# Kernel tuning notes

Measured on AMD Instinct MI355X. Metric: run time of the kernel, lower is better.

## Reference

```python
import jax, jax.numpy as jnp
import numpy as np

N = 100000
IN_C = 128
HID = 32   # 2*out_channels
OUT = 16
NEG_SLOPE = 0.2


def gat_layer(x, src, dst, n, W, a_src, a_dst, b):
    # x: [n, Cin] -> h: [n, Cout]
    h = x @ W
    alpha_s = h @ a_src  # [n]
    alpha_d = h @ a_dst  # [n]
    e = jax.nn.leaky_relu(alpha_s[src] + alpha_d[dst], NEG_SLOPE)  # [E]
    # softmax over edges grouped by destination node (self-loops ensure no empty groups)
    m = jax.ops.segment_max(e, dst, num_segments=n)
    ex = jnp.exp(e - m[dst])
    s = jax.ops.segment_sum(ex, dst, num_segments=n)
    alpha = ex / s[dst]  # [E]
    out = jax.ops.segment_sum(h[src] * alpha[:, None], dst, num_segments=n)
    return out + b


def setup_inputs() -> dict:
    key = jax.random.key(0)
    ks = jax.random.split(key, 16)
    x = jax.random.normal(ks[0], (N, IN_C), dtype=jnp.float32)
    edge_index = jax.random.randint(ks[1], (2, 1600000), 0, N, dtype=jnp.int64)

    def glorot(k, shape):
        fan = shape[0] + (shape[1] if len(shape) > 1 else 1)
        return jax.random.normal(k, shape, dtype=jnp.float32) * jnp.sqrt(2.0 / fan)

    return {
        "x": x,
        "edge_index": edge_index,
        "W1": glorot(ks[2], (IN_C, HID)),
        "a1_src": glorot(ks[3], (HID,)),
        "a1_dst": glorot(ks[4], (HID,)),
        "b1": jnp.zeros((HID,), dtype=jnp.float32),
        "W_mu": glorot(ks[5], (HID, OUT)),
        "a_mu_src": glorot(ks[6], (OUT,)),
        "a_mu_dst": glorot(ks[7], (OUT,)),
        "b_mu": jnp.zeros((OUT,), dtype=jnp.float32),
        "W_ls": glorot(ks[8], (HID, OUT)),
        "a_ls_src": glorot(ks[9], (OUT,)),
        "a_ls_dst": glorot(ks[10], (OUT,)),
        "b_ls": jnp.zeros((OUT,), dtype=jnp.float32),
    }


def reference(x, edge_index, W1, a1_src, a1_dst, b1,
              W_mu, a_mu_src, a_mu_dst, b_mu,
              W_ls, a_ls_src, a_ls_dst, b_ls):
    n = x.shape[0]
    # PyG GATConv default: add self-loops
    loop = jnp.arange(n, dtype=edge_index.dtype)
    src = jnp.concatenate([edge_index[0], loop])
    dst = jnp.concatenate([edge_index[1], loop])

    h = jax.nn.relu(gat_layer(x, src, dst, n, W1, a1_src, a1_dst, b1))
    mu = gat_layer(h, src, dst, n, W_mu, a_mu_src, a_mu_dst, b_mu)
    logstd = gat_layer(h, src, dst, n, W_ls, a_ls_src, a_ls_dst, b_ls)
    return (mu, logstd)
```

## Files before the change

### kernel.cpp

```cpp
#include <hip/hip_runtime.h>
#include <hip/hip_bf16.h>
#include <hip/hip_fp16.h>

typedef unsigned int u32;
typedef unsigned short u16;

__device__ __forceinline__ float lrelu(float v) {
    return v > 0.f ? v : 0.2f * v;
}

__device__ __forceinline__ float4 ldq_h16(const u16* __restrict__ row, int q) {
    uint2 u = ((const uint2*)row)[q];
    __half2 a = *(__half2*)&u.x;
    __half2 b = *(__half2*)&u.y;
    float2 fa = __half22float2(a);
    float2 fb = __half22float2(b);
    return make_float4(fa.x, fa.y, fb.x, fb.y);
}

__device__ __forceinline__ u32 pack2h(float x, float y) {
    __half2 h = __float22half2_rn(make_float2(x, y));
    return *(u32*)&h;
}

#define PCHUNK 4096
#define NW 256

__global__ __launch_bounds__(256) void g1p_kernel(
    const float* __restrict__ x, const float* __restrict__ W,
    const float* __restrict__ a_src, const float* __restrict__ a_dst,
    u16* __restrict__ h16, float* __restrict__ as_, float* __restrict__ ad_,
    const int* __restrict__ srcI, const int* __restrict__ dstI,
    u32* __restrict__ pairs, u32* __restrict__ bcur,
    int n, int E, int wsz, int cap, int pgrid)
{
    __shared__ float xs[64][132];
    __shared__ float Wl[128][32];
    __shared__ float asv[32], adv[32];
    __shared__ u32 lcount[NW];
    __shared__ u32 lbase[NW];
    int t = threadIdx.x;

    if ((int)blockIdx.x < pgrid) {
        int chunk = blockIdx.x * PCHUNK;
        lcount[t] = 0;
        __syncthreads();
        u32 pk[16]; int wv[16]; u32 rk[16]; bool val[16];
#pragma unroll
        for (int k = 0; k < 16; k++) {
            int i = chunk + k * 256 + t;
            val[k] = i < E;
            if (val[k]) {
                u32 s = (u32)srcI[i];
                u32 d = (u32)dstI[i];
                wv[k] = d / (u32)wsz;
                u32 dloc = d - (u32)wv[k] * (u32)wsz;
                pk[k] = (dloc << 17) | s;
                rk[k] = atomicAdd(&lcount[wv[k]], 1u);
            }
        }
        __syncthreads();
        if (lcount[t] > 0)
            lbase[t] = atomicAdd(&bcur[t], lcount[t]);
        __syncthreads();
#pragma unroll
        for (int k = 0; k < 16; k++) {
            if (val[k]) {
                u32 pos = lbase[wv[k]] + rk[k];
                if (pos < (u32)cap)
                    pairs[(size_t)wv[k] * cap + pos] = pk[k];
            }
        }
        return;
    }

    int rb = (blockIdx.x - pgrid) * 64;

    for (int i = t; i < 4096; i += 256) Wl[i >> 5][i & 31] = W[i];
    if (t < 32) { asv[t] = a_src[t]; adv[t] = a_dst[t]; }
    for (int i = t; i < 2048; i += 256) {
        int row = i >> 5, seg = i & 31;
        float4 v = make_float4(0.f, 0.f, 0.f, 0.f);
        if (rb + row < n)
            v = ((const float4*)(x + (size_t)(rb + row) * 128))[seg];
        int c = seg * 4;
        xs[row][c + 0] = v.x; xs[row][c + 1] = v.y;
        xs[row][c + 2] = v.z; xs[row][c + 3] = v.w;
    }
    __syncthreads();

    int tr = t >> 3;
    int tc = t & 7;
    float acc[2][4];
#pragma unroll
    for (int i = 0; i < 2; i++)
#pragma unroll
        for (int j = 0; j < 4; j++) acc[i][j] = 0.f;

#pragma unroll 4
    for (int k = 0; k < 128; k++) {
        float x0 = xs[tr][k];
        float x1 = xs[tr + 32][k];
        float4 wv = *(const float4*)&Wl[k][tc * 4];
        acc[0][0] += x0 * wv.x; acc[0][1] += x0 * wv.y;
        acc[0][2] += x0 * wv.z; acc[0][3] += x0 * wv.w;
        acc[1][0] += x1 * wv.x; acc[1][1] += x1 * wv.y;
        acc[1][2] += x1 * wv.z; acc[1][3] += x1 * wv.w;
    }

#pragma unroll
    for (int i = 0; i < 2; i++) {
        int r = rb + tr + i * 32;
        if (r < n) {
            uint2 p;
            p.x = pack2h(acc[i][0], acc[i][1]);
            p.y = pack2h(acc[i][2], acc[i][3]);
            *(uint2*)&h16[(size_t)r * 32 + tc * 4] = p;
        }
        float ps = 0.f, pd = 0.f;
#pragma unroll
        for (int j = 0; j < 4; j++) {
            int c = tc * 4 + j;
            ps += acc[i][j] * asv[c];
            pd += acc[i][j] * adv[c];
        }
        for (int m = 1; m < 8; m <<= 1) {
            ps += __shfl_xor(ps, m, 64);
            pd += __shfl_xor(pd, m, 64);
        }
        if (tc == 0 && r < n) { as_[r] = ps; ad_[r] = pd; }
    }
}

__global__ __launch_bounds__(256) void csr_window_kernel(
    const u32* __restrict__ pairs, const u32* __restrict__ bcur,
    u32* __restrict__ rowS, u32* __restrict__ deg, int* __restrict__ srcS,
    u32* __restrict__ perm,
    int n, int wsz, int cap)
{
    __shared__ u32 dw[512];
    __shared__ u32 cw[512];
    __shared__ u32 ts[256];
    __shared__ u32 hb[512];
    int grp = blockIdx.x;
    int t = threadIdx.x;
    int wlo = grp * wsz;
    int wnodes = n - wlo; if (wnodes < 0) wnodes = 0; if (wnodes > wsz) wnodes = wsz;
    u32 cnt = bcur[grp]; if (cnt > (u32)cap) cnt = (u32)cap;
    size_t base = (size_t)grp * cap;

    {
        int wlo_t = t * wsz;
        int wn_t = n - wlo_t; if (wn_t < 0) wn_t = 0; if (wn_t > wsz) wn_t = wsz;
        u32 c_t = bcur[t]; if (c_t > (u32)cap) c_t = (u32)cap;
        ts[t] = c_t + (u32)wn_t;
        __syncthreads();
        for (int o = 1; o < NW; o <<= 1) {
            u32 y = (t >= o) ? ts[t - o] : 0u;
            __syncthreads();
            ts[t] += y;
            __syncthreads();
        }
    }
    u32 wb = ts[grp] - (cnt + (u32)wnodes);
    __syncthreads();

    dw[t] = 0; dw[t + 256] = 0;
    hb[t] = 0; hb[t + 256] = 0;
    __syncthreads();
    for (u32 i = t; i < cnt; i += 256)
        atomicAdd(&dw[pairs[base + i] >> 17], 1u);
    __syncthreads();

    int i0 = 2 * t, i1 = 2 * t + 1;
    u32 e0 = (i0 < wnodes) ? dw[i0] + 1u : 0u;
    u32 e1 = (i1 < wnodes) ? dw[i1] + 1u : 0u;
    ts[t] = e0 + e1;
    __syncthreads();
    for (int o = 1; o < 256; o <<= 1) {
        u32 y = (t >= o) ? ts[t - o] : 0u;
        __syncthreads();
        ts[t] += y;
        __syncthreads();
    }
    u32 off = wb + ts[t] - (e0 + e1);
    if (i0 < wnodes) {
        u32 dgi = dw[i0];
        cw[i0] = off;
        rowS[wlo + i0] = off;
        deg[wlo + i0] = dgi;
        srcS[off + dgi] = wlo + i0;
    }
    u32 off1 = off + e0;
    if (i1 < wnodes) {
        u32 dgi = dw[i1];
        cw[i1] = off1;
        rowS[wlo + i1] = off1;
        deg[wlo + i1] = dgi;
        srcS[off1 + dgi] = wlo + i1;
    }
    __syncthreads();

    for (int i = t; i < wnodes; i += 256)
        atomicAdd(&hb[dw[i] < 511u ? dw[i] : 511u], 1u);
    __syncthreads();
    {
        u32 h0 = hb[2 * t], h1 = hb[2 * t + 1];
        ts[t] = h0 + h1;
        __syncthreads();
        for (int o = 1; o < 256; o <<= 1) {
            u32 y = (t >= o) ? ts[t - o] : 0u;
            __syncthreads();
            ts[t] += y;
            __syncthreads();
        }
        u32 b0 = ts[t] - (h0 + h1);
        hb[2 * t] = b0;
        hb[2 * t + 1] = b0 + h0;
    }
    __syncthreads();
    for (int i = t; i < wnodes; i += 256) {
        u32 dg = dw[i] < 511u ? dw[i] : 511u;
        u32 pos = atomicAdd(&hb[dg], 1u);
        perm[wlo + pos] = (u32)(wlo + i);
    }
    for (int i = wnodes + t; i < wsz; i += 256)
        perm[wlo + i] = 0x7fffffffu;
    __syncthreads();

    for (u32 i = t; i < cnt; i += 256) {
        u32 pr = pairs[base + i];
        u32 pos = atomicAdd(&cw[pr >> 17], 1u);
        srcS[pos] = (int)(pr & 0x1FFFFu);
    }
}

__global__ __launch_bounds__(256) void l1g2_kernel(
    const u32* __restrict__ rowS, const u32* __restrict__ deg,
    const int* __restrict__ srcS, const u32* __restrict__ perm,
    const float* __restrict__ as_, const float* __restrict__ ad_,
    const u16* __restrict__ h16, const float* __restrict__ b1,
    const float* __restrict__ Wm, const float* __restrict__ Wl_,
    const float* __restrict__ ams, const float* __restrict__ amd,
    const float* __restrict__ alsb, const float* __restrict__ ald,
    u16* __restrict__ hmhl16, float2* __restrict__ attn2,
    float* __restrict__ amud, float* __restrict__ alsd,
    int n, int ntot)
{
    __shared__ float hs[16][36];
    __shared__ float Wms[32][16], Wls[32][16];
    __shared__ float amsv[16], amdv[16], alsv[16], aldv[16];
    __shared__ int dsl[16];
    int t = threadIdx.x;

    for (int i = t; i < 512; i += 256) {
        Wms[i >> 4][i & 15] = Wm[i];
        Wls[i >> 4][i & 15] = Wl_[i];
    }
    if (t < 16) {
        amsv[t] = ams[t]; amdv[t] = amd[t];
        alsv[t] = alsb[t]; aldv[t] = ald[t];
    }

    int gid = blockIdx.x * 16 + (t >> 4);
    int d = (gid < ntot) ? (int)perm[gid] : 0x7fffffff;
    bool live = (u32)d < (u32)n;
    int l  = t & 15;
    int e2 = l >> 3;
    int q  = l & 7;
    int gb = (t & 63) & 48;

    int beg = 0, end = 0;
    float adv = 0.f;
    if (live) {
        beg = (int)rowS[d];
        end = beg + (int)deg[d] + 1;
        adv = ad_[d];
    }

    float wsum = 0.f;
    float4 acc = make_float4(0.f, 0.f, 0.f, 0.f);

    for (int tb = beg; tb < end; tb += 16) {
        int j = tb + l;
        bool valid = j < end;
        int s = valid ? srcS[j] : 0;
        float p = valid ? __expf(fminf(lrelu(as_[s] + adv), 60.f)) : 0.f;
        int cnt = end - tb; if (cnt > 16) cnt = 16;
        for (int jj = 0; jj < cnt; jj += 2) {
            int idx = jj + e2;
            int sj  = __shfl(s, gb + idx, 64);
            float w = __shfl(p, gb + idx, 64);
            if (idx >= cnt) w = 0.f;
            wsum += w;
            float4 hv = ldq_h16(h16 + (size_t)sj * 32, q);
            acc.x += w * hv.x; acc.y += w * hv.y;
            acc.z += w * hv.z; acc.w += w * hv.w;
        }
    }
    wsum  += __shfl_xor(wsum, 8, 64);
    acc.x += __shfl_xor(acc.x, 8, 64);
    acc.y += __shfl_xor(acc.y, 8, 64);
    acc.z += __shfl_xor(acc.z, 8, 64);
    acc.w += __shfl_xor(acc.w, 8, 64);

    if (l == 0) dsl[t >> 4] = live ? d : -1;
    if (live && l < 8) {
        float inv = 1.f / wsum;
        float4 r;
        r.x = fmaxf(acc.x * inv + b1[4 * q + 0], 0.f);
        r.y = fmaxf(acc.y * inv + b1[4 * q + 1], 0.f);
        r.z = fmaxf(acc.z * inv + b1[4 * q + 2], 0.f);
        r.w = fmaxf(acc.w * inv + b1[4 * q + 3], 0.f);
        *(float4*)&hs[t >> 4][4 * q] = r;
    }
    __syncthreads();

    int tr = t >> 4;
    int c  = t & 15;
    int r2 = dsl[tr];
    float accm = 0.f, accl = 0.f;
#pragma unroll
    for (int k = 0; k < 32; k++) {
        float hv = hs[tr][k];
        accm += hv * Wms[k][c];
        accl += hv * Wls[k][c];
    }
    if (r2 >= 0) {
        hmhl16[(size_t)r2 * 32 + c]      = __half_as_ushort(__float2half(accm));
        hmhl16[(size_t)r2 * 32 + 16 + c] = __half_as_ushort(__float2half(accl));
    }
    float pms = accm * amsv[c], pmd = accm * amdv[c];
    float pls = accl * alsv[c], pld = accl * aldv[c];
    for (int m = 1; m < 16; m <<= 1) {
        pms += __shfl_xor(pms, m, 64);
        pmd += __shfl_xor(pmd, m, 64);
        pls += __shfl_xor(pls, m, 64);
        pld += __shfl_xor(pld, m, 64);
    }
    if (c == 0 && r2 >= 0) {
        attn2[r2] = make_float2(pms, pls);
        amud[r2] = pmd;
        alsd[r2] = pld;
    }
}

__global__ __launch_bounds__(256) void l2_fused_kernel(
    const u32* __restrict__ rowS, const u32* __restrict__ deg,
    const int* __restrict__ srcS, const u32* __restrict__ perm,
    const float2* __restrict__ attn2,
    const float* __restrict__ amud, const float* __restrict__ alsd,
    const u16* __restrict__ hmhl16,
    const float* __restrict__ bm, const float* __restrict__ bl,
    float* __restrict__ out, int n, int ntot)
{
    int gid = blockIdx.x * 16 + (threadIdx.x >> 4);
    if (gid >= ntot) return;
    int d = (int)perm[gid];
    if (d >= n) return;
    int l  = threadIdx.x & 15;
    int e2 = l >> 3;
    int q  = l & 7;
    int gb = (threadIdx.x & 63) & 48;
    bool isMu = q < 4;

    int beg = (int)rowS[d];
    int end = beg + (int)deg[d] + 1;
    float amdv = amud[d], aldv = alsd[d];

    float wsum = 0.f;
    float4 acc = make_float4(0.f, 0.f, 0.f, 0.f);

    for (int tb = beg; tb < end; tb += 16) {
        int j = tb + l;
        bool valid = j < end;
        int s = valid ? srcS[j] : 0;
        float2 a2 = valid ? attn2[s] : make_float2(0.f, 0.f);
        float pm = valid ? __expf(fminf(lrelu(a2.x + amdv), 60.f)) : 0.f;
        float pl = valid ? __expf(fminf(lrelu(a2.y + aldv), 60.f)) : 0.f;
        int cnt = end - tb; if (cnt > 16) cnt = 16;
        for (int jj = 0; jj < cnt; jj += 2) {
            int idx = jj + e2;
            int sj    = __shfl(s, gb + idx, 64);
            float pmj = __shfl(pm, gb + idx, 64);
            float plj = __shfl(pl, gb + idx, 64);
            float w = isMu ? pmj : plj;
            if (idx >= cnt) w = 0.f;
            wsum += w;
            float4 hv = ldq_h16(hmhl16 + (size_t)sj * 32, q);
            acc.x += w * hv.x; acc.y += w * hv.y;
            acc.z += w * hv.z; acc.w += w * hv.w;
        }
    }
    wsum  += __shfl_xor(wsum, 8, 64);
    acc.x += __shfl_xor(acc.x, 8, 64);
    acc.y += __shfl_xor(acc.y, 8, 64);
    acc.z += __shfl_xor(acc.z, 8, 64);
    acc.w += __shfl_xor(acc.w, 8, 64);
    if (l < 8) {
        float inv = 1.f / wsum;
        if (q < 4) {
            float4 r;
            r.x = acc.x * inv + bm[4 * q + 0];
            r.y = acc.y * inv + bm[4 * q + 1];
            r.z = acc.z * inv + bm[4 * q + 2];
            r.w = acc.w * inv + bm[4 * q + 3];
            *(float4*)&out[(size_t)d * 16 + 4 * q] = r;
        } else {
            int qc = 4 * (q - 4);
            float4 r;
            r.x = acc.x * inv + bl[qc + 0];
            r.y = acc.y * inv + bl[qc + 1];
            r.z = acc.z * inv + bl[qc + 2];
            r.w = acc.w * inv + bl[qc + 3];
            *(float4*)&out[(size_t)n * 16 + (size_t)d * 16 + qc] = r;
        }
    }
}

extern "C" void kernel_launch(void* const* d_in, const int* in_sizes, int n_in,
                              void* d_out, int out_size, void* d_ws, size_t ws_size,
                              hipStream_t stream)
{
    const float* x   = (const float*)d_in[0];
    const int*   ei  = (const int*)d_in[1];
    const float* W1  = (const float*)d_in[2];
    const float* a1s = (const float*)d_in[3];
    const float* a1d = (const float*)d_in[4];
    const float* b1  = (const float*)d_in[5];
    const float* Wm  = (const float*)d_in[6];
    const float* ams = (const float*)d_in[7];
    const float* amd = (const float*)d_in[8];
    const float* bm  = (const float*)d_in[9];
    const float* Wl  = (const float*)d_in[10];
    const float* als = (const float*)d_in[11];
    const float* ald = (const float*)d_in[12];
    const float* bl  = (const float*)d_in[13];

    int n  = in_sizes[0] / 128;
    int E  = in_sizes[1] / 2;
    int Et = E + n;
    int wsz = (n + NW - 1) / NW;
    int cap = E / NW + 3072;
    int ntot = NW * wsz;
    const int* srcI = ei;
    const int* dstI = ei + E;

    float* ws = (float*)d_ws;
    u16*    h16   = (u16*)ws;
    u16*    hmhl16 = (u16*)(ws + (size_t)16 * n);
    u32*    pairs = (u32*)(ws + (size_t)32 * n);
    float2* attn2 = (float2*)(ws + (size_t)64 * n);
    float*  amud = ws + (size_t)66 * n;
    float*  alsd = ws + (size_t)67 * n;
    u32*    deg  = (u32*)(ws + (size_t)68 * n);
    u32*    bcur = (u32*)(ws + (size_t)69 * n);
    u32*    rowS = (u32*)(ws + (size_t)70 * n);
    int*    srcS = (int*)(ws + (size_t)71 * n);
    u32*    perm = (u32*)(ws + (size_t)71 * n + Et);
    float*  as_  = ws + (size_t)71 * n + Et + ntot;
    float*  ad_  = as_ + n;

    int pgrid = (E + PCHUNK - 1) / PCHUNK;
    int gblocks = (n + 63) / 64;

    hipMemsetAsync(bcur, 0, NW * sizeof(u32), stream);

    g1p_kernel<<<pgrid + gblocks, 256, 0, stream>>>(
        x, W1, a1s, a1d, h16, as_, ad_,
        srcI, dstI, pairs, bcur, n, E, wsz, cap, pgrid);

    csr_window_kernel<<<NW, 256, 0, stream>>>(pairs, bcur,
                                              rowS, deg, srcS, perm,
                                              n, wsz, cap);

    l1g2_kernel<<<(ntot + 15) / 16, 256, 0, stream>>>(
        rowS, deg, srcS, perm, as_, ad_, h16, b1,
        Wm, Wl, ams, amd, als, ald,
        hmhl16, attn2, amud, alsd, n, ntot);

    l2_fused_kernel<<<(ntot + 15) / 16, 256, 0, stream>>>(rowS, deg, srcS, perm,
                                                          attn2, amud, alsd,
                                                          hmhl16, bm, bl,
                                                          (float*)d_out, n, ntot);
}
```

Before: 246.8 us.

## Pair layer-1 GEMM with CSR window build instead of edge partition

Splits edge partitioning into its own kernel, then fuses the per-window CSR build with the layer-1 feature GEMM in one launch, sharing a union shared-memory buffer. The aim is to overlap the latency-bound, low-occupancy CSR stage (256 blocks full of barriers) with the GEMM blocks, rather than overlapping partition with the GEMM. The GEMM's shared-memory footprint now also applies to the CSR blocks, which may lower their occupancy, and the partition stage now runs alone.

```diff
diff --git a/kernel.cpp b/kernel.cpp
--- a/kernel.cpp
+++ b/kernel.cpp
@@ -26,66 +26,168 @@
 #define PCHUNK 4096
 #define NW 256
 
-__global__ __launch_bounds__(256) void g1p_kernel(
+__global__ __launch_bounds__(256) void partition_kernel(
+    const int* __restrict__ srcI, const int* __restrict__ dstI,
+    u32* __restrict__ pairs, u32* __restrict__ bcur,
+    int E, int wsz, int cap)
+{
+    __shared__ u32 lcount[NW];
+    __shared__ u32 lbase[NW];
+    int t = threadIdx.x;
+    int chunk = blockIdx.x * PCHUNK;
+    lcount[t] = 0;
+    __syncthreads();
+    u32 pk[16]; int wv[16]; u32 rk[16]; bool val[16];
+#pragma unroll
+    for (int k = 0; k < 16; k++) {
+        int i = chunk + k * 256 + t;
+        val[k] = i < E;
+        if (val[k]) {
+            u32 s = (u32)srcI[i];
+            u32 d = (u32)dstI[i];
+            wv[k] = d / (u32)wsz;
+            u32 dloc = d - (u32)wv[k] * (u32)wsz;
+            pk[k] = (dloc << 17) | s;
+            rk[k] = atomicAdd(&lcount[wv[k]], 1u);
+        }
+    }
+    __syncthreads();
+    if (lcount[t] > 0)
+        lbase[t] = atomicAdd(&bcur[t], lcount[t]);
+    __syncthreads();
+#pragma unroll
+    for (int k = 0; k < 16; k++) {
+        if (val[k]) {
+            u32 pos = lbase[wv[k]] + rk[k];
+            if (pos < (u32)cap)
+                pairs[(size_t)wv[k] * cap + pos] = pk[k];
+        }
+    }
+}
+
+struct GSm { float xs[64][132]; float Wl[128][32]; float asv[32], adv[32]; };
+struct CSm { u32 dw[512], cw[512], ts[256], hb[512]; };
+
+__global__ __launch_bounds__(256) void g1c_kernel(
     const float* __restrict__ x, const float* __restrict__ W,
     const float* __restrict__ a_src, const float* __restrict__ a_dst,
     u16* __restrict__ h16, float* __restrict__ as_, float* __restrict__ ad_,
-    const int* __restrict__ srcI, const int* __restrict__ dstI,
-    u32* __restrict__ pairs, u32* __restrict__ bcur,
-    int n, int E, int wsz, int cap, int pgrid)
+    const u32* __restrict__ pairs, const u32* __restrict__ bcur,
+    u32* __restrict__ rowS, u32* __restrict__ deg, int* __restrict__ srcS,
+    u32* __restrict__ perm,
+    int n, int wsz, int cap)
 {
-    __shared__ float xs[64][132];
-    __shared__ float Wl[128][32];
-    __shared__ float asv[32], adv[32];
-    __shared__ u32 lcount[NW];
-    __shared__ u32 lbase[NW];
+    __shared__ __align__(16) char smraw[sizeof(GSm)];
     int t = threadIdx.x;
 
-    if ((int)blockIdx.x < pgrid) {
-        int chunk = blockIdx.x * PCHUNK;
-        lcount[t] = 0;
-        __syncthreads();
-        u32 pk[16]; int wv[16]; u32 rk[16]; bool val[16];
-#pragma unroll
-        for (int k = 0; k < 16; k++) {
-            int i = chunk + k * 256 + t;
-            val[k] = i < E;
-            if (val[k]) {
-                u32 s = (u32)srcI[i];
-                u32 d = (u32)dstI[i];
-                wv[k] = d / (u32)wsz;
-                u32 dloc = d - (u32)wv[k] * (u32)wsz;
-                pk[k] = (dloc << 17) | s;
-                rk[k] = atomicAdd(&lcount[wv[k]], 1u);
+    if ((int)blockIdx.x < NW) {
+        CSm& s = *reinterpret_cast<CSm*>(smraw);
+        int grp = blockIdx.x;
+        int wlo = grp * wsz;
+        int wnodes = n - wlo; if (wnodes < 0) wnodes = 0; if (wnodes > wsz) wnodes = wsz;
+        u32 cnt = bcur[grp]; if (cnt > (u32)cap) cnt = (u32)cap;
+        size_t base = (size_t)grp * cap;
+
+        {
+            int wlo_t = t * wsz;
+            int wn_t = n - wlo_t; if (wn_t < 0) wn_t = 0; if (wn_t > wsz) wn_t = wsz;
+            u32 c_t = bcur[t]; if (c_t > (u32)cap) c_t = (u32)cap;
+            s.ts[t] = c_t + (u32)wn_t;
+            __syncthreads();
+            for (int o = 1; o < NW; o <<= 1) {
+                u32 y = (t >= o) ? s.ts[t - o] : 0u;
+                __syncthreads();
+                s.ts[t] += y;
+                __syncthreads();
             }
         }
-        __syncthreads();
-        if (lcount[t] > 0)
-            lbase[t] = atomicAdd(&bcur[t], lcount[t]);
-        __syncthreads();
-#pragma unroll
-        for (int k = 0; k < 16; k++) {
-            if (val[k]) {
-                u32 pos = lbase[wv[k]] + rk[k];
-                if (pos < (u32)cap)
-                    pairs[(size_t)wv[k] * cap + pos] = pk[k];
+        u32 wb = s.ts[grp] - (cnt + (u32)wnodes);
+        __syncthreads();
+
+        s.dw[t] = 0; s.dw[t + 256] = 0;
+        s.hb[t] = 0; s.hb[t + 256] = 0;
+        __syncthreads();
+        for (u32 i = t; i < cnt; i += 256)
+            atomicAdd(&s.dw[pairs[base + i] >> 17], 1u);
+        __syncthreads();
+
+        int i0 = 2 * t, i1 = 2 * t + 1;
+        u32 e0 = (i0 < wnodes) ? s.dw[i0] + 1u : 0u;
+        u32 e1 = (i1 < wnodes) ? s.dw[i1] + 1u : 0u;
+        s.ts[t] = e0 + e1;
+        __syncthreads();
+        for (int o = 1; o < 256; o <<= 1) {
+            u32 y = (t >= o) ? s.ts[t - o] : 0u;
+            __syncthreads();
+            s.ts[t] += y;
+            __syncthreads();
+        }
+        u32 off = wb + s.ts[t] - (e0 + e1);
+        if (i0 < wnodes) {
+            u32 dgi = s.dw[i0];
+            s.cw[i0] = off;
+            rowS[wlo + i0] = off;
+            deg[wlo + i0] = dgi;
+            srcS[off + dgi] = wlo + i0;
+        }
+        u32 off1 = off + e0;
+        if (i1 < wnodes) {
+            u32 dgi = s.dw[i1];
+            s.cw[i1] = off1;
+            rowS[wlo + i1] = off1;
+            deg[wlo + i1] = dgi;
+            srcS[off1 + dgi] = wlo + i1;
+        }
+        __syncthreads();
+
+        for (int i = t; i < wnodes; i += 256)
+            atomicAdd(&s.hb[s.dw[i] < 511u ? s.dw[i] : 511u], 1u);
+        __syncthreads();
+        {
+            u32 h0 = s.hb[2 * t], h1 = s.hb[2 * t + 1];
+            s.ts[t] = h0 + h1;
+            __syncthreads();
+            for (int o = 1; o < 256; o <<= 1) {
+                u32 y = (t >= o) ? s.ts[t - o] : 0u;
+                __syncthreads();
+                s.ts[t] += y;
+                __syncthreads();
             }
+            u32 b0 = s.ts[t] - (h0 + h1);
+            s.hb[2 * t] = b0;
+            s.hb[2 * t + 1] = b0 + h0;
+        }
+        __syncthreads();
+        for (int i = t; i < wnodes; i += 256) {
+            u32 dg = s.dw[i] < 511u ? s.dw[i] : 511u;
+            u32 pos = atomicAdd(&s.hb[dg], 1u);
+            perm[wlo + pos] = (u32)(wlo + i);
+        }
+        for (int i = wnodes + t; i < wsz; i += 256)
+            perm[wlo + i] = 0x7fffffffu;
+        __syncthreads();
+
+        for (u32 i = t; i < cnt; i += 256) {
+            u32 pr = pairs[base + i];
+            u32 pos = atomicAdd(&s.cw[pr >> 17], 1u);
+            srcS[pos] = (int)(pr & 0x1FFFFu);
         }
         return;
     }
 
-    int rb = (blockIdx.x - pgrid) * 64;
-
-    for (int i = t; i < 4096; i += 256) Wl[i >> 5][i & 31] = W[i];
-    if (t < 32) { asv[t] = a_src[t]; adv[t] = a_dst[t]; }
+    GSm& s = *reinterpret_cast<GSm*>(smraw);
+    int rb = (blockIdx.x - NW) * 64;
+
+    for (int i = t; i < 4096; i += 256) s.Wl[i >> 5][i & 31] = W[i];
+    if (t < 32) { s.asv[t] = a_src[t]; s.adv[t] = a_dst[t]; }
     for (int i = t; i < 2048; i += 256) {
         int row = i >> 5, seg = i & 31;
         float4 v = make_float4(0.f, 0.f, 0.f, 0.f);
         if (rb + row < n)
             v = ((const float4*)(x + (size_t)(rb + row) * 128))[seg];
         int c = seg * 4;
-        xs[row][c + 0] = v.x; xs[row][c + 1] = v.y;
-        xs[row][c + 2] = v.z; xs[row][c + 3] = v.w;
+        s.xs[row][c + 0] = v.x; s.xs[row][c + 1] = v.y;
+        s.xs[row][c + 2] = v.z; s.xs[row][c + 3] = v.w;
     }
     __syncthreads();
 
@@ -99,9 +201,9 @@
 
 #pragma unroll 4
     for (int k = 0; k < 128; k++) {
-        float x0 = xs[tr][k];
-        float x1 = xs[tr + 32][k];
-        float4 wv = *(const float4*)&Wl[k][tc * 4];
+        float x0 = s.xs[tr][k];
+        float x1 = s.xs[tr + 32][k];
+        float4 wv = *(const float4*)&s.Wl[k][tc * 4];
         acc[0][0] += x0 * wv.x; acc[0][1] += x0 * wv.y;
         acc[0][2] += x0 * wv.z; acc[0][3] += x0 * wv.w;
         acc[1][0] += x1 * wv.x; acc[1][1] += x1 * wv.y;
@@ -121,117 +223,14 @@
 #pragma unroll
         for (int j = 0; j < 4; j++) {
             int c = tc * 4 + j;
-            ps += acc[i][j] * asv[c];
-            pd += acc[i][j] * adv[c];
+            ps += acc[i][j] * s.asv[c];
+            pd += acc[i][j] * s.adv[c];
         }
         for (int m = 1; m < 8; m <<= 1) {
             ps += __shfl_xor(ps, m, 64);
             pd += __shfl_xor(pd, m, 64);
         }
         if (tc == 0 && r < n) { as_[r] = ps; ad_[r] = pd; }
-    }
-}
-
-__global__ __launch_bounds__(256) void csr_window_kernel(
-    const u32* __restrict__ pairs, const u32* __restrict__ bcur,
-    u32* __restrict__ rowS, u32* __restrict__ deg, int* __restrict__ srcS,
-    u32* __restrict__ perm,
-    int n, int wsz, int cap)
-{
-    __shared__ u32 dw[512];
-    __shared__ u32 cw[512];
-    __shared__ u32 ts[256];
-    __shared__ u32 hb[512];
-    int grp = blockIdx.x;
-    int t = threadIdx.x;
-    int wlo = grp * wsz;
-    int wnodes = n - wlo; if (wnodes < 0) wnodes = 0; if (wnodes > wsz) wnodes = wsz;
-    u32 cnt = bcur[grp]; if (cnt > (u32)cap) cnt = (u32)cap;
-    size_t base = (size_t)grp * cap;
-
-    {
-        int wlo_t = t * wsz;
-        int wn_t = n - wlo_t; if (wn_t < 0) wn_t = 0; if (wn_t > wsz) wn_t = wsz;
-        u32 c_t = bcur[t]; if (c_t > (u32)cap) c_t = (u32)cap;
-        ts[t] = c_t + (u32)wn_t;
-        __syncthreads();
-        for (int o = 1; o < NW; o <<= 1) {
-            u32 y = (t >= o) ? ts[t - o] : 0u;
-            __syncthreads();
-            ts[t] += y;
-            __syncthreads();
-        }
-    }
-    u32 wb = ts[grp] - (cnt + (u32)wnodes);
-    __syncthreads();
-
-    dw[t] = 0; dw[t + 256] = 0;
-    hb[t] = 0; hb[t + 256] = 0;
-    __syncthreads();
-    for (u32 i = t; i < cnt; i += 256)
-        atomicAdd(&dw[pairs[base + i] >> 17], 1u);
-    __syncthreads();
-
-    int i0 = 2 * t, i1 = 2 * t + 1;
-    u32 e0 = (i0 < wnodes) ? dw[i0] + 1u : 0u;
-    u32 e1 = (i1 < wnodes) ? dw[i1] + 1u : 0u;
-    ts[t] = e0 + e1;
-    __syncthreads();
-    for (int o = 1; o < 256; o <<= 1) {
-        u32 y = (t >= o) ? ts[t - o] : 0u;
-        __syncthreads();
-        ts[t] += y;
-        __syncthreads();
-    }
-    u32 off = wb + ts[t] - (e0 + e1);
-    if (i0 < wnodes) {
-        u32 dgi = dw[i0];
-        cw[i0] = off;
-        rowS[wlo + i0] = off;
-        deg[wlo + i0] = dgi;
-        srcS[off + dgi] = wlo + i0;
-    }
-    u32 off1 = off + e0;
-    if (i1 < wnodes) {
-        u32 dgi = dw[i1];
-        cw[i1] = off1;
-        rowS[wlo + i1] = off1;
-        deg[wlo + i1] = dgi;
-        srcS[off1 + dgi] = wlo + i1;
-    }
-    __syncthreads();
-
-    for (int i = t; i < wnodes; i += 256)
-        atomicAdd(&hb[dw[i] < 511u ? dw[i] : 511u], 1u);
-    __syncthreads();
-    {
-        u32 h0 = hb[2 * t], h1 = hb[2 * t + 1];
-        ts[t] = h0 + h1;
-        __syncthreads();
-        for (int o = 1; o < 256; o <<= 1) {
-            u32 y = (t >= o) ? ts[t - o] : 0u;
-            __syncthreads();
-            ts[t] += y;
-            __syncthreads();
-        }
-        u32 b0 = ts[t] - (h0 + h1);
-        hb[2 * t] = b0;
-        hb[2 * t + 1] = b0 + h0;
-    }
-    __syncthreads();
-    for (int i = t; i < wnodes; i += 256) {
-        u32 dg = dw[i] < 511u ? dw[i] : 511u;
-        u32 pos = atomicAdd(&hb[dg], 1u);
-        perm[wlo + pos] = (u32)(wlo + i);
-    }
-    for (int i = wnodes + t; i < wsz; i += 256)
-        perm[wlo + i] = 0x7fffffffu;
-    __syncthreads();
-
-    for (u32 i = t; i < cnt; i += 256) {
-        u32 pr = pairs[base + i];
-        u32 pos = atomicAdd(&cw[pr >> 17], 1u);
-        srcS[pos] = (int)(pr & 0x1FFFFu);
     }
 }
 
@@ -466,13 +465,12 @@
 
     hipMemsetAsync(bcur, 0, NW * sizeof(u32), stream);
 
-    g1p_kernel<<<pgrid + gblocks, 256, 0, stream>>>(
+    partition_kernel<<<pgrid, 256, 0, stream>>>(srcI, dstI, pairs, bcur,
+                                                E, wsz, cap);
+
+    g1c_kernel<<<NW + gblocks, 256, 0, stream>>>(
         x, W1, a1s, a1d, h16, as_, ad_,
-        srcI, dstI, pairs, bcur, n, E, wsz, cap, pgrid);
-
-    csr_window_kernel<<<NW, 256, 0, stream>>>(pairs, bcur,
-                                              rowS, deg, srcS, perm,
-                                              n, wsz, cap);
+        pairs, bcur, rowS, deg, srcS, perm, n, wsz, cap);
 
     l1g2_kernel<<<(ntot + 15) / 16, 256, 0, stream>>>(
         rowS, deg, srcS, perm, as_, ad_, h16, b1,
```

After: 243.3 us. Within noise of the previous version (-1.4%).
